# Performance work log

Hardware: AMD Instinct MI355X
Metric: run time of the kernel (lower is better)

Reference implementation:

```python
import jax, jax.numpy as jnp
import numpy as np

IN_F = 4096
OUT_F = 4096
N_TOK = 8192


def setup_inputs() -> dict:
    key = jax.random.key(0)
    kx, kw = jax.random.split(key)
    x = jax.random.normal(kx, (N_TOK, IN_F), dtype=jnp.float32)
    weight = jax.random.normal(kw, (OUT_F, IN_F), dtype=jnp.float32) * 0.1
    bias = jnp.zeros((OUT_F,), dtype=jnp.float32)
    return {"x": x, "weight": weight, "bias": bias}


def reference(x, weight, bias):
    # sign() maps 0 -> 0 (same as torch.sign); clamp to [-1,1] is a no-op after sign
    x_b = jnp.sign(x)
    w_b = jnp.sign(weight)
    out = x_b @ w_b.T  # [N, OUT_F]
    return out + bias
```

## Files before the change

kernel.cpp:

```cpp
#include <hip/hip_runtime.h>
#include <stdint.h>

#define NTOK 8192
#define INF  4096
#define OUTF 4096
#define KDIM 4096
#define KB4  2048

using i32x4 = __attribute__((ext_vector_type(4))) int;
using i32x8 = __attribute__((ext_vector_type(8))) int;
using f32x4 = __attribute__((ext_vector_type(4))) float;

#define GLOAD16(gp, lp) __builtin_amdgcn_global_load_lds( \
    (const __attribute__((address_space(1))) uint32_t*)(gp), \
    (__attribute__((address_space(3))) uint32_t*)(lp), 16, 0, 0)

#define SBARP()  do { __builtin_amdgcn_s_barrier(); __builtin_amdgcn_sched_barrier(0); } while (0)
#define SBARX()  __builtin_amdgcn_s_barrier()
#define VMCNT4() do { asm volatile("s_waitcnt vmcnt(4)" ::: "memory"); __builtin_amdgcn_sched_barrier(0); } while (0)
#define VMCNT0() do { asm volatile("s_waitcnt vmcnt(0)" ::: "memory"); __builtin_amdgcn_sched_barrier(0); } while (0)

__device__ __forceinline__ void full_swizzle(int orig, int& row0, int& col0) {
    const int wgid  = ((orig & 7) << 6) | (orig >> 3);
    const int chunk = wgid >> 6;
    const int c     = wgid & 63;
    row0 = ((chunk << 2) | (c & 3)) * 256;
    col0 = (c >> 2) * 256;
}

__global__ void pack_fp4(const float* __restrict__ x, const float* __restrict__ w,
                         char* __restrict__ xp, char* __restrict__ wp,
                         int gx, int gtot) {
    int gtid = blockIdx.x * blockDim.x + threadIdx.x;
    int nthr = gridDim.x * blockDim.x;
    for (int g = gtid; g < gtot; g += nthr) {
        const float* src;
        char* dst;
        int gi;
        if (g < gx) { src = x; dst = xp; gi = g; }
        else        { src = w; dst = wp; gi = g - gx; }
        const float4* s4 = reinterpret_cast<const float4*>(src + (size_t)gi * 32);
        unsigned int words[4];
#pragma unroll
        for (int wd = 0; wd < 4; ++wd) {
            float4 va = s4[wd * 2];
            float4 vb = s4[wd * 2 + 1];
            unsigned int b0 = (0x2u + ((va.x < 0.0f) ? 8u : 0u)) | ((0x2u + ((va.y < 0.0f) ? 8u : 0u)) << 4);
            unsigned int b1 = (0x2u + ((va.z < 0.0f) ? 8u : 0u)) | ((0x2u + ((va.w < 0.0f) ? 8u : 0u)) << 4);
            unsigned int b2 = (0x2u + ((vb.x < 0.0f) ? 8u : 0u)) | ((0x2u + ((vb.y < 0.0f) ? 8u : 0u)) << 4);
            unsigned int b3 = (0x2u + ((vb.z < 0.0f) ? 8u : 0u)) | ((0x2u + ((vb.w < 0.0f) ? 8u : 0u)) << 4);
            words[wd] = b0 | (b1 << 8) | (b2 << 16) | (b3 << 24);
        }
        uint4 o = make_uint4(words[0], words[1], words[2], words[3]);
        *reinterpret_cast<uint4*>(dst + (size_t)gi * 16) = o;
    }
}

__global__ __launch_bounds__(512, 2) void bgemm_fp4(
        const char*  __restrict__ Xp,
        const char*  __restrict__ Wp,
        const float* __restrict__ bias,
        float*       __restrict__ out)
{
    __shared__ __align__(16) char As[2][32768];
    __shared__ __align__(16) char Bs[2][32768];

    const int tid  = threadIdx.x;
    const int lane = tid & 63;
    const int wid  = tid >> 6;
    const int wr   = wid >> 2;
    const int wc   = wid & 3;
    const int cl   = lane & 15;
    const int rg   = lane >> 4;

    int row0, col0;
    full_swizzle(blockIdx.x, row0, col0);

    const int rr     = tid >> 3;
    const int colOff = ((tid & 7) << 4) ^ ((rr & 7) << 4);
    const char* gA = Xp + (size_t)(row0 + rr) * KB4 + colOff;
    const char* gB = Wp + (size_t)(col0 + rr) * KB4 + colOff;
    const int d0 = tid * 16;

#define STGF(arr, p, g, ktB) do { \
    GLOAD16((g) + (size_t)0   * KB4 + (ktB), &arr[p][d0]); \
    GLOAD16((g) + (size_t)64  * KB4 + (ktB), &arr[p][8192 + d0]); \
    GLOAD16((g) + (size_t)128 * KB4 + (ktB), &arr[p][16384 + d0]); \
    GLOAD16((g) + (size_t)192 * KB4 + (ktB), &arr[p][24576 + d0]); \
} while (0)

    const int aRow = (wr * 128 + cl) * 128;
    const int bRow = (wc * 64 + cl) * 128;
    const int kq0  = (rg << 4) ^ ((cl & 7) << 4);
    const int kq1  = kq0 ^ 64;

    f32x4 acc[8][4];
#pragma unroll
    for (int m = 0; m < 8; ++m)
#pragma unroll
        for (int n = 0; n < 4; ++n)
#pragma unroll
            for (int j = 0; j < 4; ++j) acc[m][n][j] = 0.0f;

    i32x4 af[4][2], bf[4][2];

#define LDA(p, MH) do { \
    _Pragma("unroll") for (int m = 0; m < 4; ++m) { \
        af[m][0] = *reinterpret_cast<const i32x4*>(&As[p][aRow + ((MH) * 4 + m) * 2048 + kq0]); \
        af[m][1] = *reinterpret_cast<const i32x4*>(&As[p][aRow + ((MH) * 4 + m) * 2048 + kq1]); \
    } } while (0)
#define LDBALL(p) do { \
    _Pragma("unroll") for (int n = 0; n < 4; ++n) { \
        bf[n][0] = *reinterpret_cast<const i32x4*>(&Bs[p][bRow + (n) * 2048 + kq0]); \
        bf[n][1] = *reinterpret_cast<const i32x4*>(&Bs[p][bRow + (n) * 2048 + kq1]); \
    } } while (0)
#define MMALL(MH) do { \
    __builtin_amdgcn_s_setprio(1); \
    _Pragma("unroll") for (int kk = 0; kk < 2; ++kk) \
    _Pragma("unroll") for (int m = 0; m < 4; ++m) \
    _Pragma("unroll") for (int n = 0; n < 4; ++n) { \
        i32x8 a8 = {af[m][kk][0], af[m][kk][1], af[m][kk][2], af[m][kk][3], 0, 0, 0, 0}; \
        i32x8 b8 = {bf[n][kk][0], bf[n][kk][1], bf[n][kk][2], bf[n][kk][3], 0, 0, 0, 0}; \
        acc[(MH) * 4 + m][n] = __builtin_amdgcn_mfma_scale_f32_16x16x128_f8f6f4( \
            a8, b8, acc[(MH) * 4 + m][n], 4, 4, 0, 0x7F7F7F7F, 0, 0x7F7F7F7F); \
    } \
    __builtin_amdgcn_s_setprio(0); \
} while (0)

    STGF(As, 0, gA, 0);
    STGF(Bs, 0, gB, 0);
    STGF(Bs, 1, gB, 128);
    VMCNT4();
    SBARX();

    int kb = 0;
#pragma unroll 1
    for (int i = 0; i < 7; ++i, kb += 256) {
        LDA(0, 0); LDBALL(0);
        STGF(As, 1, gA, kb + 128);
        SBARP(); MMALL(0); SBARX();
        LDA(0, 1);
        STGF(Bs, 0, gB, kb + 256);
        SBARP(); MMALL(1);
        VMCNT4(); SBARX();
        LDA(1, 0); LDBALL(1);
        STGF(As, 0, gA, kb + 256);
        SBARP(); MMALL(0); SBARX();
        LDA(1, 1);
        STGF(Bs, 1, gB, kb + 384);
        SBARP(); MMALL(1);
        VMCNT4(); SBARX();
    }

    STGF(As, 1, gA, 1920);
    VMCNT0();
    SBARX();
    LDA(0, 0); LDBALL(0); MMALL(0);
    LDA(0, 1);            MMALL(1);
    LDA(1, 0); LDBALL(1); MMALL(0);
    LDA(1, 1);            MMALL(1);

    float bv[4];
#pragma unroll
    for (int n = 0; n < 4; ++n) bv[n] = bias[col0 + wc * 64 + n * 16 + cl];

#pragma unroll
    for (int m = 0; m < 8; ++m) {
        int rowbase = row0 + wr * 128 + m * 16 + rg * 4;
#pragma unroll
        for (int j = 0; j < 4; ++j) {
            size_t rb = (size_t)(rowbase + j) * OUTF;
#pragma unroll
            for (int n = 0; n < 4; ++n) {
                int col = col0 + wc * 64 + n * 16 + cl;
                out[rb + col] = acc[m][n][j] + bv[n];
            }
        }
    }
#undef STGF
#undef LDA
#undef LDBALL
#undef MMALL
}

__global__ void pack_i8(const float* __restrict__ x, const float* __restrict__ w,
                        char* __restrict__ xp, char* __restrict__ wp,
                        int gx, int gtot) {
    int gtid = blockIdx.x * blockDim.x + threadIdx.x;
    int nthr = gridDim.x * blockDim.x;
    for (int g = gtid; g < gtot; g += nthr) {
        const float* src;
        char* dst;
        int gi;
        if (g < gx) { src = x; dst = xp; gi = g; }
        else        { src = w; dst = wp; gi = g - gx; }
        const float4* s4 = reinterpret_cast<const float4*>(src + (size_t)gi * 16);
        int words[4];
#pragma unroll
        for (int q = 0; q < 4; ++q) {
            float4 v = s4[q];
            int b0 = (v.x < 0.0f) ? 0xFF : 0x01;
            int b1 = (v.y < 0.0f) ? 0xFF : 0x01;
            int b2 = (v.z < 0.0f) ? 0xFF : 0x01;
            int b3 = (v.w < 0.0f) ? 0xFF : 0x01;
            words[q] = b0 | (b1 << 8) | (b2 << 16) | (b3 << 24);
        }
        int4 o = make_int4(words[0], words[1], words[2], words[3]);
        *reinterpret_cast<int4*>(dst + (size_t)gi * 16) = o;
    }
}

__global__ __launch_bounds__(512, 2) void bgemm_i8_4ph(
        const char*  __restrict__ Xp, const char* __restrict__ Wp,
        const float* __restrict__ bias, float* __restrict__ out)
{
    __shared__ __align__(16) char As[2][32768];
    __shared__ __align__(16) char Bs[2][32768];

    const int tid  = threadIdx.x;
    const int lane = tid & 63;
    const int wid  = tid >> 6;
    const int wr   = wid >> 2;
    const int wc   = wid & 3;
    const int cl   = lane & 15;
    const int rg   = lane >> 4;

    int row0, col0;
    full_swizzle(blockIdx.x, row0, col0);

    const int rr     = tid >> 3;
    const int colOff = ((tid & 7) << 4) ^ ((rr & 7) << 4);
    const char* gA = Xp + (size_t)(row0 + rr) * KDIM + colOff;
    const char* gB = Wp + (size_t)(col0 + rr) * KDIM + colOff;
    const int d0 = tid * 16;

#define STGF(arr, p, g, ktB) do { \
    GLOAD16((g) + (size_t)0   * KDIM + (ktB), &arr[p][d0]); \
    GLOAD16((g) + (size_t)64  * KDIM + (ktB), &arr[p][8192 + d0]); \
    GLOAD16((g) + (size_t)128 * KDIM + (ktB), &arr[p][16384 + d0]); \
    GLOAD16((g) + (size_t)192 * KDIM + (ktB), &arr[p][24576 + d0]); \
} while (0)

    const int aRow = (wr * 128 + cl) * 128;
    const int bRow = (wc * 64 + cl) * 128;
    const int kq0  = (rg << 4) ^ ((cl & 7) << 4);
    const int kq1  = kq0 ^ 64;

    i32x4 acc[8][4];
#pragma unroll
    for (int m = 0; m < 8; ++m)
#pragma unroll
        for (int n = 0; n < 4; ++n)
#pragma unroll
            for (int j = 0; j < 4; ++j) acc[m][n][j] = 0;

    i32x4 af[4][2], bf[4][2];

#define LDA(p, MH) do { \
    _Pragma("unroll") for (int m = 0; m < 4; ++m) { \
        af[m][0] = *reinterpret_cast<const i32x4*>(&As[p][aRow + ((MH) * 4 + m) * 2048 + kq0]); \
        af[m][1] = *reinterpret_cast<const i32x4*>(&As[p][aRow + ((MH) * 4 + m) * 2048 + kq1]); \
    } } while (0)
#define LDBALL(p) do { \
    _Pragma("unroll") for (int n = 0; n < 4; ++n) { \
        bf[n][0] = *reinterpret_cast<const i32x4*>(&Bs[p][bRow + (n) * 2048 + kq0]); \
        bf[n][1] = *reinterpret_cast<const i32x4*>(&Bs[p][bRow + (n) * 2048 + kq1]); \
    } } while (0)
#define MMALL(MH) do { \
    __builtin_amdgcn_s_setprio(1); \
    _Pragma("unroll") for (int m = 0; m < 4; ++m) \
    _Pragma("unroll") for (int n = 0; n < 4; ++n) \
    _Pragma("unroll") for (int kk = 0; kk < 2; ++kk) \
        acc[(MH) * 4 + m][n] = __builtin_amdgcn_mfma_i32_16x16x64_i8( \
            af[m][kk], bf[n][kk], acc[(MH) * 4 + m][n], 0, 0, 0); \
    __builtin_amdgcn_s_setprio(0); \
} while (0)

    STGF(As, 0, gA, 0);
    STGF(Bs, 0, gB, 0);
    STGF(Bs, 1, gB, 128);
    VMCNT4();
    SBARX();

    int kb = 0;
#pragma unroll 1
    for (int i = 0; i < 15; ++i, kb += 256) {
        LDA(0, 0); LDBALL(0);
        STGF(As, 1, gA, kb + 128);
        SBARP(); MMALL(0); SBARX();
        LDA(0, 1);
        STGF(Bs, 0, gB, kb + 256);
        SBARP(); MMALL(1);
        VMCNT4(); SBARX();
        LDA(1, 0); LDBALL(1);
        STGF(As, 0, gA, kb + 256);
        SBARP(); MMALL(0); SBARX();
        LDA(1, 1);
        STGF(Bs, 1, gB, kb + 384);
        SBARP(); MMALL(1);
        VMCNT4(); SBARX();
    }

    STGF(As, 1, gA, 3968);
    VMCNT0();
    SBARX();
    LDA(0, 0); LDBALL(0); MMALL(0);
    LDA(0, 1);            MMALL(1);
    LDA(1, 0); LDBALL(1); MMALL(0);
    LDA(1, 1);            MMALL(1);

    float bv[4];
#pragma unroll
    for (int n = 0; n < 4; ++n) bv[n] = bias[col0 + wc * 64 + n * 16 + cl];

#pragma unroll
    for (int m = 0; m < 8; ++m) {
        int rowbase = row0 + wr * 128 + m * 16 + rg * 4;
#pragma unroll
        for (int j = 0; j < 4; ++j) {
            size_t rb = (size_t)(rowbase + j) * OUTF;
#pragma unroll
            for (int n = 0; n < 4; ++n) {
                int col = col0 + wc * 64 + n * 16 + cl;
                out[rb + col] = (float)acc[m][n][j] + bv[n];
            }
        }
    }
#undef STGF
#undef LDA
#undef LDBALL
#undef MMALL
}

#define KW   64
#define LSTRIDE 66

__global__ void pack_both_fb(const float* __restrict__ x, const float* __restrict__ w,
                             uint64_t* __restrict__ xp, uint64_t* __restrict__ wp,
                             int nx, int ntot) {
    int gtid  = blockIdx.x * blockDim.x + threadIdx.x;
    int lane  = threadIdx.x & 63;
    int wave  = gtid >> 6;
    int nwaves = (gridDim.x * blockDim.x) >> 6;
    for (int q = wave; q < ntot; q += nwaves) {
        const float* src; uint64_t* dst; int qi;
        if (q < nx) { src = x; dst = xp; qi = q; }
        else        { src = w; dst = wp; qi = q - nx; }
        float v = src[(size_t)qi * 64 + lane];
        unsigned long long m = __ballot(v < 0.0f);
        if (lane == 0) dst[qi] = (uint64_t)m;
    }
}

__global__ __launch_bounds__(512, 2) void bgemm_popc_fb(
        const uint64_t* __restrict__ xp, const uint64_t* __restrict__ wp,
        const float* __restrict__ bias, float* __restrict__ out)
{
    __shared__ uint64_t xs[128 * LSTRIDE];
    __shared__ uint64_t ws[128 * LSTRIDE];
    const int tid  = threadIdx.x;
    const int row0 = blockIdx.y * 128;
    const int col0 = blockIdx.x * 128;
    {
        const uint64_t* xg = xp + (size_t)row0 * KW;
        const uint64_t* wg = wp + (size_t)col0 * KW;
#pragma unroll
        for (int m = 0; m < 8; ++m) {
            int q = (m * 512 + tid) * 2;
            int r = q >> 6;
            int k = q & 63;
            ulonglong2 vx = *reinterpret_cast<const ulonglong2*>(xg + q);
            xs[r * LSTRIDE + k] = vx.x; xs[r * LSTRIDE + k + 1] = vx.y;
            ulonglong2 vw = *reinterpret_cast<const ulonglong2*>(wg + q);
            ws[r * LSTRIDE + k] = vw.x; ws[r * LSTRIDE + k + 1] = vw.y;
        }
    }
    __syncthreads();
    const int tx = tid & 15;
    const int ty = tid >> 4;
    int acc[4][8];
#pragma unroll
    for (int i = 0; i < 4; ++i)
#pragma unroll
        for (int j = 0; j < 8; ++j) acc[i][j] = 0;
    const uint64_t* xrow = xs + ty * 4 * LSTRIDE;
    const uint64_t* wrow = ws + tx * LSTRIDE;
#pragma unroll 4
    for (int kk = 0; kk < KW; kk += 2) {
        ulonglong2 a[4]; ulonglong2 b[8];
#pragma unroll
        for (int i = 0; i < 4; ++i)
            a[i] = *reinterpret_cast<const ulonglong2*>(xrow + i * LSTRIDE + kk);
#pragma unroll
        for (int j = 0; j < 8; ++j)
            b[j] = *reinterpret_cast<const ulonglong2*>(wrow + j * 16 * LSTRIDE + kk);
#pragma unroll
        for (int i = 0; i < 4; ++i)
#pragma unroll
            for (int j = 0; j < 8; ++j)
                acc[i][j] += __builtin_popcountll(a[i].x ^ b[j].x)
                           + __builtin_popcountll(a[i].y ^ b[j].y);
    }
    float bcol[8];
#pragma unroll
    for (int j = 0; j < 8; ++j) bcol[j] = bias[col0 + tx + 16 * j];
#pragma unroll
    for (int i = 0; i < 4; ++i) {
        size_t r = (size_t)(row0 + ty * 4 + i);
#pragma unroll
        for (int j = 0; j < 8; ++j) {
            int c = col0 + tx + 16 * j;
            out[r * OUTF + c] = (float)(INF - 2 * acc[i][j]) + bcol[j];
        }
    }
}

extern "C" void kernel_launch(void* const* d_in, const int* in_sizes, int n_in,
                              void* d_out, int out_size, void* d_ws, size_t ws_size,
                              hipStream_t stream) {
    const float* x    = (const float*)d_in[0];
    const float* w    = (const float*)d_in[1];
    const float* bias = (const float*)d_in[2];
    float* out = (float*)d_out;

    const size_t need4 = (size_t)NTOK * KB4 + (size_t)OUTF * KB4;
    const size_t need8 = (size_t)NTOK * KDIM + (size_t)OUTF * KDIM;

    if (ws_size >= need4) {
        char* xp = (char*)d_ws;
        char* wp = xp + (size_t)NTOK * KB4;
        const int gx   = NTOK * KDIM / 32;
        const int gtot = gx + OUTF * KDIM / 32;
        pack_fp4<<<2048, 256, 0, stream>>>(x, w, xp, wp, gx, gtot);
        bgemm_fp4<<<512, 512, 0, stream>>>(xp, wp, bias, out);
    } else if (ws_size >= need8) {
        char* xp = (char*)d_ws;
        char* wp = xp + (size_t)NTOK * KDIM;
        const int gx   = NTOK * KDIM / 16;
        const int gtot = gx + OUTF * KDIM / 16;
        pack_i8<<<2048, 256, 0, stream>>>(x, w, xp, wp, gx, gtot);
        bgemm_i8_4ph<<<512, 512, 0, stream>>>(xp, wp, bias, out);
    } else {
        uint64_t* xp = (uint64_t*)d_ws;
        uint64_t* wp = xp + (size_t)NTOK * KW;
        const int nx   = NTOK * KW;
        const int ntot = nx + OUTF * KW;
        pack_both_fb<<<2048, 256, 0, stream>>>(x, w, xp, wp, nx, ntot);
        dim3 grid(OUTF / 128, NTOK / 128);
        bgemm_popc_fb<<<grid, 512, 0, stream>>>(xp, wp, bias, out);
    }
}
```

Measured before the change: 131.5 us.

## Remove pre-MFMA barriers and repack FP4 with one float4 per thread

The main loops of both GEMM kernels drop the barrier that sat between the LDS fragment loads and the MFMA block, keeping one scheduling-fenced barrier after each compute phase. This cuts one workgroup-wide sync per phase and lets MFMAs start without waiting on other waves, but it relies on the remaining barriers and vmcnt waits to keep the LDS double buffering race-free. The FP4 pack kernel also changes so each thread converts one float4 into a 16-bit store instead of 32 floats into a 16-byte store. That gives coalesced loads across threads but uses narrow 2-byte writes and many more loop iterations.

```diff
diff --git a/kernel.cpp b/kernel.cpp
--- a/kernel.cpp
+++ b/kernel.cpp
@@ -15,8 +15,7 @@
     (const __attribute__((address_space(1))) uint32_t*)(gp), \
     (__attribute__((address_space(3))) uint32_t*)(lp), 16, 0, 0)
 
-#define SBARP()  do { __builtin_amdgcn_s_barrier(); __builtin_amdgcn_sched_barrier(0); } while (0)
-#define SBARX()  __builtin_amdgcn_s_barrier()
+#define SBARE()  do { __builtin_amdgcn_s_barrier(); __builtin_amdgcn_sched_barrier(0); } while (0)
 #define VMCNT4() do { asm volatile("s_waitcnt vmcnt(4)" ::: "memory"); __builtin_amdgcn_sched_barrier(0); } while (0)
 #define VMCNT0() do { asm volatile("s_waitcnt vmcnt(0)" ::: "memory"); __builtin_amdgcn_sched_barrier(0); } while (0)
 
@@ -30,29 +29,21 @@
 
 __global__ void pack_fp4(const float* __restrict__ x, const float* __restrict__ w,
                          char* __restrict__ xp, char* __restrict__ wp,
-                         int gx, int gtot) {
+                         int gx4, int gtot4) {
     int gtid = blockIdx.x * blockDim.x + threadIdx.x;
     int nthr = gridDim.x * blockDim.x;
-    for (int g = gtid; g < gtot; g += nthr) {
-        const float* src;
-        char* dst;
+    for (int g = gtid; g < gtot4; g += nthr) {
+        const float4* s;
+        uint16_t* d;
         int gi;
-        if (g < gx) { src = x; dst = xp; gi = g; }
-        else        { src = w; dst = wp; gi = g - gx; }
-        const float4* s4 = reinterpret_cast<const float4*>(src + (size_t)gi * 32);
-        unsigned int words[4];
-#pragma unroll
-        for (int wd = 0; wd < 4; ++wd) {
-            float4 va = s4[wd * 2];
-            float4 vb = s4[wd * 2 + 1];
-            unsigned int b0 = (0x2u + ((va.x < 0.0f) ? 8u : 0u)) | ((0x2u + ((va.y < 0.0f) ? 8u : 0u)) << 4);
-            unsigned int b1 = (0x2u + ((va.z < 0.0f) ? 8u : 0u)) | ((0x2u + ((va.w < 0.0f) ? 8u : 0u)) << 4);
-            unsigned int b2 = (0x2u + ((vb.x < 0.0f) ? 8u : 0u)) | ((0x2u + ((vb.y < 0.0f) ? 8u : 0u)) << 4);
-            unsigned int b3 = (0x2u + ((vb.z < 0.0f) ? 8u : 0u)) | ((0x2u + ((vb.w < 0.0f) ? 8u : 0u)) << 4);
-            words[wd] = b0 | (b1 << 8) | (b2 << 16) | (b3 << 24);
-        }
-        uint4 o = make_uint4(words[0], words[1], words[2], words[3]);
-        *reinterpret_cast<uint4*>(dst + (size_t)gi * 16) = o;
+        if (g < gx4) { s = (const float4*)x; d = (uint16_t*)xp; gi = g; }
+        else         { s = (const float4*)w; d = (uint16_t*)wp; gi = g - gx4; }
+        float4 v = s[gi];
+        unsigned int n0 = 0x2u | ((v.x < 0.0f) ? 8u : 0u);
+        unsigned int n1 = 0x2u | ((v.y < 0.0f) ? 8u : 0u);
+        unsigned int n2 = 0x2u | ((v.z < 0.0f) ? 8u : 0u);
+        unsigned int n3 = 0x2u | ((v.w < 0.0f) ? 8u : 0u);
+        d[gi] = (uint16_t)(n0 | (n1 << 4) | (n2 << 8) | (n3 << 12));
     }
 }
 
@@ -131,30 +122,32 @@
     STGF(Bs, 0, gB, 0);
     STGF(Bs, 1, gB, 128);
     VMCNT4();
-    SBARX();
+    SBARE();
 
     int kb = 0;
 #pragma unroll 1
     for (int i = 0; i < 7; ++i, kb += 256) {
         LDA(0, 0); LDBALL(0);
         STGF(As, 1, gA, kb + 128);
-        SBARP(); MMALL(0); SBARX();
+        MMALL(0);
+        SBARE();
         LDA(0, 1);
         STGF(Bs, 0, gB, kb + 256);
-        SBARP(); MMALL(1);
-        VMCNT4(); SBARX();
+        MMALL(1);
+        VMCNT4(); SBARE();
         LDA(1, 0); LDBALL(1);
         STGF(As, 0, gA, kb + 256);
-        SBARP(); MMALL(0); SBARX();
+        MMALL(0);
+        SBARE();
         LDA(1, 1);
         STGF(Bs, 1, gB, kb + 384);
-        SBARP(); MMALL(1);
-        VMCNT4(); SBARX();
+        MMALL(1);
+        VMCNT4(); SBARE();
     }
 
     STGF(As, 1, gA, 1920);
     VMCNT0();
-    SBARX();
+    SBARE();
     LDA(0, 0); LDBALL(0); MMALL(0);
     LDA(0, 1);            MMALL(1);
     LDA(1, 0); LDBALL(1); MMALL(0);
@@ -280,30 +273,32 @@
     STGF(Bs, 0, gB, 0);
     STGF(Bs, 1, gB, 128);
     VMCNT4();
-    SBARX();
+    SBARE();
 
     int kb = 0;
 #pragma unroll 1
     for (int i = 0; i < 15; ++i, kb += 256) {
         LDA(0, 0); LDBALL(0);
         STGF(As, 1, gA, kb + 128);
-        SBARP(); MMALL(0); SBARX();
+        MMALL(0);
+        SBARE();
         LDA(0, 1);
         STGF(Bs, 0, gB, kb + 256);
-        SBARP(); MMALL(1);
-        VMCNT4(); SBARX();
+        MMALL(1);
+        VMCNT4(); SBARE();
         LDA(1, 0); LDBALL(1);
         STGF(As, 0, gA, kb + 256);
-        SBARP(); MMALL(0); SBARX();
+        MMALL(0);
+        SBARE();
         LDA(1, 1);
         STGF(Bs, 1, gB, kb + 384);
-        SBARP(); MMALL(1);
-        VMCNT4(); SBARX();
+        MMALL(1);
+        VMCNT4(); SBARE();
     }
 
     STGF(As, 1, gA, 3968);
     VMCNT0();
-    SBARX();
+    SBARE();
     LDA(0, 0); LDBALL(0); MMALL(0);
     LDA(0, 1);            MMALL(1);
     LDA(1, 0); LDBALL(1); MMALL(0);
@@ -429,9 +424,9 @@
     if (ws_size >= need4) {
         char* xp = (char*)d_ws;
         char* wp = xp + (size_t)NTOK * KB4;
-        const int gx   = NTOK * KDIM / 32;
-        const int gtot = gx + OUTF * KDIM / 32;
-        pack_fp4<<<2048, 256, 0, stream>>>(x, w, xp, wp, gx, gtot);
+        const int gx4   = NTOK * KDIM / 4;
+        const int gtot4 = gx4 + OUTF * KDIM / 4;
+        pack_fp4<<<2048, 256, 0, stream>>>(x, w, xp, wp, gx4, gtot4);
         bgemm_fp4<<<512, 512, 0, stream>>>(xp, wp, bias, out);
     } else if (ws_size >= need8) {
         char* xp = (char*)d_ws;
```

Measured after the change: 131.0 us. No clear change (-0.4%).
